# Optimization experiments

Measured on AMD Instinct MI355X. Metric: run time of the kernel, lower is better.

## Reference

```python
import jax, jax.numpy as jnp
import numpy as np

N_NODES = 100000
D = 128        # hidden_channels
H = 64         # hidden_size
E = 8192       # num_hyperedges
K = 32         # nodes per hyperedge (fixed group size)


def setup_inputs() -> dict:
    key = jax.random.key(0)
    k1, k2, k3, k4, k5, k6 = jax.random.split(key, 6)
    X = jax.random.normal(k1, (N_NODES, D), dtype=jnp.float32)
    idx = jax.random.randint(k2, (E, K), 0, N_NODES, dtype=jnp.int64)
    # per-hyperedge MLP params (torch Linear: y = x @ W.T + b), scaled like
    # torch's default uniform fan-in init magnitude
    W1 = jax.random.normal(k3, (E, H, D), dtype=jnp.float32) / np.sqrt(D)
    b1 = jax.random.normal(k4, (E, H), dtype=jnp.float32) / np.sqrt(D)
    W2 = jax.random.normal(k5, (E, H), dtype=jnp.float32) / np.sqrt(H)
    b2 = jax.random.normal(k6, (E,), dtype=jnp.float32) / np.sqrt(H)
    return {"X": X, "idx": idx, "W1": W1, "b1": b1, "W2": W2, "b2": b2}


def reference(X, idx, W1, b1, W2, b2):
    # gather node features per hyperedge: [E, K, D]
    x_he = X[idx]
    # per-edge 2-layer MLP scorer (leaky_relu slope 0.01 = torch default)
    h = jax.nn.leaky_relu(jnp.einsum('ekd,ehd->ekh', x_he, W1) + b1[:, None, :])
    w = jnp.einsum('ekh,eh->ek', h, W2) + b2[:, None]          # [E, K]
    beta = jax.nn.softmax(w, axis=1)                           # softmax over group
    z = jnp.einsum('ek,ekd->ed', beta, x_he)                   # weighted sum reduce
    Z = jnp.tanh(jax.nn.leaky_relu(z))                         # [E, D]
    return Z, beta
```

## Files before the change

### kernel.cpp

```cpp
#include <hip/hip_runtime.h>

#define E_EDGES 8192
#define KN 32
#define DD 128
#define HH 64

typedef __attribute__((ext_vector_type(8))) __bf16 bf16x8;
typedef __attribute__((ext_vector_type(4))) float f32x4;

__device__ __forceinline__ unsigned short f2bf(float f) {
    unsigned int u = __builtin_bit_cast(unsigned int, f);
    u += 0x7FFFu + ((u >> 16) & 1u);
    return (unsigned short)(u >> 16);
}

__global__ __launch_bounds__(256)
void he_attn_kernel(const float* __restrict__ X,
                    const int* __restrict__ idx,
                    const float* __restrict__ W1,
                    const float* __restrict__ b1,
                    const float* __restrict__ W2,
                    const float* __restrict__ b2,
                    float* __restrict__ Zout,
                    float* __restrict__ Bout)
{
    const int e   = blockIdx.x;
    const int tid = threadIdx.x;
    const int lane = tid & 63;
    const int wv   = tid >> 6;

    __shared__ float xs32[KN][DD];
    __shared__ unsigned short xsb[KN][DD + 8];
    __shared__ unsigned short wsb[HH][DD + 8];
    __shared__ float wpart[4][KN];
    __shared__ float beta_s[KN];

    #pragma unroll
    for (int it = 0; it < 4; ++it) {
        int i = tid + it * 256;
        int k = i >> 5;
        int c = i & 31;
        int row = idx[e * KN + k];
        float4 v = reinterpret_cast<const float4*>(X)[(size_t)row * (DD / 4) + c];
        *reinterpret_cast<float4*>(&xs32[k][c * 4]) = v;
        ushort4 bv;
        bv.x = f2bf(v.x); bv.y = f2bf(v.y); bv.z = f2bf(v.z); bv.w = f2bf(v.w);
        *reinterpret_cast<ushort4*>(&xsb[k][c * 4]) = bv;
    }
    const float4* W1e = reinterpret_cast<const float4*>(W1 + (size_t)e * HH * DD);
    #pragma unroll
    for (int it = 0; it < 8; ++it) {
        int i = tid + it * 256;
        int jj = i >> 5;
        int c  = i & 31;
        float4 v = W1e[i];
        ushort4 bv;
        bv.x = f2bf(v.x); bv.y = f2bf(v.y); bv.z = f2bf(v.z); bv.w = f2bf(v.w);
        *reinterpret_cast<ushort4*>(&wsb[jj][c * 4]) = bv;
    }
    __syncthreads();

    const int cl = lane & 15;
    const int kg = lane >> 4;
    f32x4 acc0 = {0.f, 0.f, 0.f, 0.f};
    f32x4 acc1 = {0.f, 0.f, 0.f, 0.f};
    #pragma unroll
    for (int kc = 0; kc < 4; ++kc) {
        const int ds = kc * 32 + kg * 8;
        bf16x8 a0 = *reinterpret_cast<const bf16x8*>(&xsb[cl][ds]);
        bf16x8 a1 = *reinterpret_cast<const bf16x8*>(&xsb[16 + cl][ds]);
        bf16x8 bb = *reinterpret_cast<const bf16x8*>(&wsb[wv * 16 + cl][ds]);
        acc0 = __builtin_amdgcn_mfma_f32_16x16x32_bf16(a0, bb, acc0, 0, 0, 0);
        acc1 = __builtin_amdgcn_mfma_f32_16x16x32_bf16(a1, bb, acc1, 0, 0, 0);
    }

    const int j = wv * 16 + cl;
    const float b1j = b1[e * HH + j];
    const float w2j = W2[e * HH + j];
    float pk[8];
    #pragma unroll
    for (int r = 0; r < 4; ++r) {
        float h0 = acc0[r] + b1j; h0 = (h0 > 0.f) ? h0 : 0.01f * h0;
        float h1 = acc1[r] + b1j; h1 = (h1 > 0.f) ? h1 : 0.01f * h1;
        pk[r]     = h0 * w2j;
        pk[4 + r] = h1 * w2j;
    }
    #pragma unroll
    for (int m = 1; m < 16; m <<= 1) {
        #pragma unroll
        for (int q = 0; q < 8; ++q) pk[q] += __shfl_xor(pk[q], m);
    }
    if (cl == 0) {
        #pragma unroll
        for (int r = 0; r < 4; ++r) {
            wpart[wv][kg * 4 + r]      = pk[r];
            wpart[wv][16 + kg * 4 + r] = pk[4 + r];
        }
    }
    __syncthreads();

    if (tid < KN) {
        float v = b2[e] + wpart[0][tid] + wpart[1][tid] + wpart[2][tid] + wpart[3][tid];
        float mx = v;
        #pragma unroll
        for (int off = 16; off >= 1; off >>= 1) mx = fmaxf(mx, __shfl_xor(mx, off));
        float ex = __expf(v - mx);
        float s = ex;
        #pragma unroll
        for (int off = 16; off >= 1; off >>= 1) s += __shfl_xor(s, off);
        float beta = ex / s;
        beta_s[tid] = beta;
        Bout[(size_t)e * KN + tid] = beta;
    }
    __syncthreads();

    if (tid < DD) {
        float z = 0.f;
        #pragma unroll
        for (int k = 0; k < KN; ++k) z += beta_s[k] * xs32[k][tid];
        z = (z > 0.f) ? z : 0.01f * z;
        Zout[(size_t)e * DD + tid] = tanhf(z);
    }
}

extern "C" void kernel_launch(void* const* d_in, const int* in_sizes, int n_in,
                              void* d_out, int out_size, void* d_ws, size_t ws_size,
                              hipStream_t stream) {
    const float* X   = (const float*)d_in[0];
    const int*   idx = (const int*)d_in[1];
    const float* W1  = (const float*)d_in[2];
    const float* b1  = (const float*)d_in[3];
    const float* W2  = (const float*)d_in[4];
    const float* b2  = (const float*)d_in[5];
    float* Zout = (float*)d_out;
    float* Bout = Zout + (size_t)E_EDGES * DD;
    (void)in_sizes; (void)n_in; (void)out_size; (void)d_ws; (void)ws_size;
    he_attn_kernel<<<dim3(E_EDGES), dim3(256), 0, stream>>>(X, idx, W1, b1, W2, b2, Zout, Bout);
}
```

Measured before the change: 70.46 us.

## Load W1 directly into registers and drop fp32 X staging in LDS

Each lane now loads its W1 row fragment straight from global memory into registers and packs it to bf16 for the MFMA B operand. This removes the shared-memory W1 tile and its extra LDS round trip. The fp32 copy of gathered X is also dropped: the weighted sum reads the bf16 LDS copy, which cuts LDS use from about 34KB to about 9KB and lets more blocks run per CU (launch bounds now request 4). The trade-off is that Z is computed from bf16-rounded X, which loses precision, and the per-lane W1 loads are less coalesced (32-byte pieces per lane).

Result: faster. 64.79 us (median of 2 runs) (-8.0%).

```diff
diff --git a/kernel.cpp b/kernel.cpp
--- a/kernel.cpp
+++ b/kernel.cpp
@@ -4,8 +4,10 @@
 #define KN 32
 #define DD 128
 #define HH 64
+#define XPAD 8
 
 typedef __attribute__((ext_vector_type(8))) __bf16 bf16x8;
+typedef __attribute__((ext_vector_type(8))) unsigned short u16x8;
 typedef __attribute__((ext_vector_type(4))) float f32x4;
 
 __device__ __forceinline__ unsigned short f2bf(float f) {
@@ -14,7 +16,14 @@
     return (unsigned short)(u >> 16);
 }
 
-__global__ __launch_bounds__(256)
+__device__ __forceinline__ bf16x8 pack_bf8(float4 a, float4 b) {
+    u16x8 u;
+    u[0] = f2bf(a.x); u[1] = f2bf(a.y); u[2] = f2bf(a.z); u[3] = f2bf(a.w);
+    u[4] = f2bf(b.x); u[5] = f2bf(b.y); u[6] = f2bf(b.z); u[7] = f2bf(b.w);
+    return __builtin_bit_cast(bf16x8, u);
+}
+
+__global__ __launch_bounds__(256, 4)
 void he_attn_kernel(const float* __restrict__ X,
                     const int* __restrict__ idx,
                     const float* __restrict__ W1,
@@ -24,16 +33,25 @@
                     float* __restrict__ Zout,
                     float* __restrict__ Bout)
 {
-    const int e   = blockIdx.x;
-    const int tid = threadIdx.x;
+    const int e    = blockIdx.x;
+    const int tid  = threadIdx.x;
     const int lane = tid & 63;
     const int wv   = tid >> 6;
+    const int cl   = lane & 15;
+    const int kg   = lane >> 4;
 
-    __shared__ float xs32[KN][DD];
-    __shared__ unsigned short xsb[KN][DD + 8];
-    __shared__ unsigned short wsb[HH][DD + 8];
+    __shared__ unsigned short xsb[KN][DD + XPAD];
     __shared__ float wpart[4][KN];
     __shared__ float beta_s[KN];
+
+    const int j = wv * 16 + cl;
+    const float* W1r = W1 + ((size_t)e * HH + j) * DD;
+    float4 wf[8];
+    #pragma unroll
+    for (int kc = 0; kc < 4; ++kc) {
+        wf[2 * kc]     = *reinterpret_cast<const float4*>(W1r + kc * 32 + kg * 8);
+        wf[2 * kc + 1] = *reinterpret_cast<const float4*>(W1r + kc * 32 + kg * 8 + 4);
+    }
 
     #pragma unroll
     for (int it = 0; it < 4; ++it) {
@@ -42,26 +60,12 @@
         int c = i & 31;
         int row = idx[e * KN + k];
         float4 v = reinterpret_cast<const float4*>(X)[(size_t)row * (DD / 4) + c];
-        *reinterpret_cast<float4*>(&xs32[k][c * 4]) = v;
         ushort4 bv;
         bv.x = f2bf(v.x); bv.y = f2bf(v.y); bv.z = f2bf(v.z); bv.w = f2bf(v.w);
         *reinterpret_cast<ushort4*>(&xsb[k][c * 4]) = bv;
     }
-    const float4* W1e = reinterpret_cast<const float4*>(W1 + (size_t)e * HH * DD);
-    #pragma unroll
-    for (int it = 0; it < 8; ++it) {
-        int i = tid + it * 256;
-        int jj = i >> 5;
-        int c  = i & 31;
-        float4 v = W1e[i];
-        ushort4 bv;
-        bv.x = f2bf(v.x); bv.y = f2bf(v.y); bv.z = f2bf(v.z); bv.w = f2bf(v.w);
-        *reinterpret_cast<ushort4*>(&wsb[jj][c * 4]) = bv;
-    }
     __syncthreads();
 
-    const int cl = lane & 15;
-    const int kg = lane >> 4;
     f32x4 acc0 = {0.f, 0.f, 0.f, 0.f};
     f32x4 acc1 = {0.f, 0.f, 0.f, 0.f};
     #pragma unroll
@@ -69,12 +73,11 @@
         const int ds = kc * 32 + kg * 8;
         bf16x8 a0 = *reinterpret_cast<const bf16x8*>(&xsb[cl][ds]);
         bf16x8 a1 = *reinterpret_cast<const bf16x8*>(&xsb[16 + cl][ds]);
-        bf16x8 bb = *reinterpret_cast<const bf16x8*>(&wsb[wv * 16 + cl][ds]);
+        bf16x8 bb = pack_bf8(wf[2 * kc], wf[2 * kc + 1]);
         acc0 = __builtin_amdgcn_mfma_f32_16x16x32_bf16(a0, bb, acc0, 0, 0, 0);
         acc1 = __builtin_amdgcn_mfma_f32_16x16x32_bf16(a1, bb, acc1, 0, 0, 0);
     }
 
-    const int j = wv * 16 + cl;
     const float b1j = b1[e * HH + j];
     const float w2j = W2[e * HH + j];
     float pk[8];
@@ -117,7 +120,11 @@
     if (tid < DD) {
         float z = 0.f;
         #pragma unroll
-        for (int k = 0; k < KN; ++k) z += beta_s[k] * xs32[k][tid];
+        for (int k = 0; k < KN; ++k) {
+            unsigned int b = xsb[k][tid];
+            float xv = __builtin_bit_cast(float, b << 16);
+            z += beta_s[k] * xv;
+        }
         z = (z > 0.f) ? z : 0.01f * z;
         Zout[(size_t)e * DD + tid] = tanhf(z);
     }
```
